# Kernel optimization log

Measured on AMD Instinct MI355X. Metric: run time of the kernel, lower is better.

Reference implementation:

```python
import jax, jax.numpy as jnp
import numpy as np

INPUT_SIZE = 2
HIDDEN = 64
NUM_CLASSES = 64
B = 4096
T = 512


def setup_inputs() -> dict:
    key = jax.random.key(0)
    ks = jax.random.split(key, 12)
    s_in = 1.0 / np.sqrt(HIDDEN)
    inp = {
        "x": jax.random.normal(ks[0], (B, INPUT_SIZE, T, 1), dtype=jnp.float32),
        # LSTMCell params (torch layout: [4H, in], gate order i,f,g,o)
        "W_ih": jax.random.uniform(ks[1], (4 * HIDDEN, INPUT_SIZE), minval=-s_in, maxval=s_in),
        "W_hh": jax.random.uniform(ks[2], (4 * HIDDEN, HIDDEN), minval=-s_in, maxval=s_in),
        "b_ih": jax.random.uniform(ks[3], (4 * HIDDEN,), minval=-s_in, maxval=s_in),
        "b_hh": jax.random.uniform(ks[4], (4 * HIDDEN,), minval=-s_in, maxval=s_in),
        # ODE cell f_node: Linear(H,H) -> Tanh -> Linear(H,H)
        "W1": jax.random.uniform(ks[5], (HIDDEN, HIDDEN), minval=-s_in, maxval=s_in),
        "b1": jax.random.uniform(ks[6], (HIDDEN,), minval=-s_in, maxval=s_in),
        "W2": jax.random.uniform(ks[7], (HIDDEN, HIDDEN), minval=-s_in, maxval=s_in),
        "b2": jax.random.uniform(ks[8], (HIDDEN,), minval=-s_in, maxval=s_in),
        # output projection fc
        "Wf": jax.random.uniform(ks[9], (NUM_CLASSES, HIDDEN), minval=-s_in, maxval=s_in),
        "bf": jax.random.uniform(ks[10], (NUM_CLASSES,), minval=-s_in, maxval=s_in),
    }
    return inp


def reference(x, W_ih, W_hh, b_ih, b_hh, W1, b1, W2, b2, Wf, bf):
    # x: [B, input_size, T, 1] -> [T, B, input_size] for scan over time
    xs = jnp.transpose(x[..., 0], (2, 0, 1))
    b = xs.shape[1]
    H = W_hh.shape[1]
    dt = jnp.float32(1.0 / 3.0)  # ts = ones(B), 3 fixed Euler steps of ts/3

    def f_node(h):
        return jnp.tanh(h @ W1.T + b1) @ W2.T + b2

    def step(carry, xt):
        h, c = carry
        gates = xt @ W_ih.T + h @ W_hh.T + (b_ih + b_hh)  # [B, 4H]
        i, f, g, o = jnp.split(gates, 4, axis=-1)
        c = jax.nn.sigmoid(f) * c + jax.nn.sigmoid(i) * jnp.tanh(g)
        h = jax.nn.sigmoid(o) * jnp.tanh(c)
        # fixed-Euler ODE solve: 3 steps
        for _ in range(3):
            h = h + dt * f_node(h)
        return (h, c), h @ Wf.T + bf

    h0 = jnp.zeros((b, H), dtype=x.dtype)
    c0 = jnp.zeros((b, H), dtype=x.dtype)
    _, outs = jax.lax.scan(step, (h0, c0), xs)  # outs: [T, B, num_classes]
    return jnp.transpose(outs, (1, 0, 2))  # [B, T, num_classes]
```

## Files before the change

kernel.cpp:

```cpp
#include <hip/hip_runtime.h>


#define TT 512
#define DT 0.33333334f

#define OFF_M  0
#define OFF_N  4096
#define OFF_P  20480
#define OFF_K1 24576
#define OFF_CG 24640
#define OFF_C2 24896

typedef _Float16 half8 __attribute__((ext_vector_type(8)));
typedef float f32x4 __attribute__((ext_vector_type(4)));

__device__ __forceinline__ float fsig(float x) {
  return __builtin_amdgcn_rcpf(1.0f + __expf(-x));
}
__device__ __forceinline__ float ftanh(float x) {
  return 2.0f * __builtin_amdgcn_rcpf(1.0f + __expf(-2.0f * x)) - 1.0f;
}

__global__ void prep(const float* __restrict__ Whh, const float* __restrict__ W1,
                     const float* __restrict__ W2, const float* __restrict__ b2,
                     const float* __restrict__ Wf, const float* __restrict__ bf,
                     float* __restrict__ ws) {
  int id = (int)blockIdx.x * 256 + (int)threadIdx.x;
  if (id < 4096) {
    int j = id >> 6, k = id & 63;
    float s = 0.f;
    for (int l = 0; l < 64; ++l) s += W1[j * 64 + l] * W2[l * 64 + k];
    ws[OFF_M + id] = DT * s;
  } else if (id < 20480) {
    int e = id - 4096; int gr = e >> 6, k = e & 63;
    float s = 0.f;
    for (int l = 0; l < 64; ++l) s += Whh[gr * 64 + l] * W2[l * 64 + k];
    ws[OFF_N + e] = DT * s;
  } else if (id < 24576) {
    int e = id - 20480; int j = e >> 6, k = e & 63;
    float s = 0.f;
    for (int l = 0; l < 64; ++l) s += Wf[j * 64 + l] * W2[l * 64 + k];
    ws[OFF_P + e] = DT * s;
  } else if (id < 24640) {
    int j = id - 24576;
    float s = 0.f;
    for (int l = 0; l < 64; ++l) s += W1[j * 64 + l] * b2[l];
    ws[OFF_K1 + j] = DT * s;
  } else if (id < 24896) {
    int gr = id - 24640;
    float s = 0.f;
    for (int l = 0; l < 64; ++l) s += Whh[gr * 64 + l] * b2[l];
    ws[OFF_CG + gr] = 3.0f * DT * s;
  } else if (id < 24960) {
    int j = id - 24896;
    float s = 0.f;
    for (int l = 0; l < 64; ++l) s += Wf[j * 64 + l] * b2[l];
    ws[OFF_C2 + j] = 3.0f * DT * s + bf[j];
  }
}

__device__ __forceinline__ half8 rdA(const _Float16* plane, int off) {
  return *(const half8*)(plane + off);
}

__global__ void __launch_bounds__(256, 2)
odelstm(const float* __restrict__ X, const float* __restrict__ Wih,
        const float* __restrict__ Whh, const float* __restrict__ bih,
        const float* __restrict__ bhh, const float* __restrict__ W1,
        const float* __restrict__ b1, const float* __restrict__ Wf,
        const float* __restrict__ ws, float* __restrict__ OUT)
{
  __shared__ __align__(16) _Float16 sh[5 * 1024];

  const int tid = (int)threadIdx.x;
  const int w = tid >> 6;
  const int l = tid & 63;
  const int q = l >> 4;
  const int p = l & 15;
  const int j = (w << 4) | p;
  const int row0 = (int)blockIdx.x << 3;

  half8 Bhh[4][2], Bw1[2], Bm[2], Bn[4][2], Bp[2], Bof[2];
  #pragma unroll
  for (int g = 0; g < 4; ++g) {
    #pragma unroll
    for (int kt = 0; kt < 2; ++kt) {
      const float* s  = Whh + ((g << 6) | j) * 64 + (kt << 5) + (q << 3);
      const float* sn = ws + OFF_N + (((g << 6) | j) << 6) + (kt << 5) + (q << 3);
      half8 v, vn;
      #pragma unroll
      for (int i = 0; i < 8; ++i) { v[i] = (_Float16)s[i]; vn[i] = (_Float16)sn[i]; }
      Bhh[g][kt] = v; Bn[g][kt] = vn;
    }
  }
  #pragma unroll
  for (int kt = 0; kt < 2; ++kt) {
    const float* s1 = W1 + j * 64 + (kt << 5) + (q << 3);
    const float* sm = ws + OFF_M + (j << 6) + (kt << 5) + (q << 3);
    const float* sp = ws + OFF_P + (j << 6) + (kt << 5) + (q << 3);
    const float* sf = Wf + j * 64 + (kt << 5) + (q << 3);
    half8 v1, vm, vp, vf;
    #pragma unroll
    for (int i = 0; i < 8; ++i) {
      v1[i] = (_Float16)s1[i]; vm[i] = (_Float16)sm[i];
      vp[i] = (_Float16)sp[i]; vf[i] = (_Float16)sf[i];
    }
    Bw1[kt] = v1; Bm[kt] = vm; Bp[kt] = vp; Bof[kt] = vf;
  }

  float bias0[4], biasL[4], wx0[4], wx1[4];
  #pragma unroll
  for (int g = 0; g < 4; ++g) {
    int gr = (g << 6) | j;
    bias0[g] = bih[gr] + bhh[gr];
    biasL[g] = bias0[g] + ws[OFF_CG + gr];
    wx0[g] = Wih[gr * 2];
    wx1[g] = Wih[gr * 2 + 1];
  }
  const float b1c = b1[j];
  const float k1c = ws[OFF_K1 + j];
  const float c2c = ws[OFF_C2 + j];

  int waddr[2];
  #pragma unroll
  for (int r = 0; r < 2; ++r) {
    int row = (q << 2) | r;
    waddr[r] = row * 64 + (((j >> 3) ^ (row & 7)) << 3) + (j & 7);
  }
  int roff0 = p * 64 + (((q) ^ (p & 7)) << 3);
  int roff1 = p * 64 + (((4 | q) ^ (p & 7)) << 3);

  const float* xp[2];
  float* outp[2];
  #pragma unroll
  for (int r = 0; r < 2; ++r) {
    int rb = row0 + ((q << 1) | r);
    xp[r]   = X + rb * 2 * TT;
    outp[r] = OUT + (rb * TT) * 64 + j;
  }

  for (int i = tid; i < 5 * 1024; i += 256) sh[i] = (_Float16)0.f;

  float x0[2], x1[2];
  #pragma unroll
  for (int r = 0; r < 2; ++r) { x0[r] = xp[r][0]; x1[r] = xp[r][TT]; }

  f32x4 acc[4];
  #pragma unroll
  for (int g = 0; g < 4; ++g) {
    acc[g][0] = bias0[g] + x0[0] * wx0[g] + x1[0] * wx1[g];
    acc[g][1] = bias0[g] + x0[1] * wx0[g] + x1[1] * wx1[g];
    acc[g][2] = 0.f; acc[g][3] = 0.f;
  }

  float c[2] = {0.f, 0.f};

  __syncthreads();

  for (int t = 0; t < TT; ++t) {
    _Float16* Hpl = sh + ((t & 1) << 10);
    _Float16* T0p = sh + 2048;
    _Float16* T1p = sh + 3072;
    _Float16* Spp = sh + 4096;

    #pragma unroll
    for (int r = 0; r < 2; ++r) {
      float ig = fsig(acc[0][r]);
      float fg = fsig(acc[1][r]);
      float gg = ftanh(acc[2][r]);
      float og = fsig(acc[3][r]);
      c[r] = fg * c[r] + ig * gg;
      float hv = og * ftanh(c[r]);
      Hpl[waddr[r]] = (_Float16)hv;
    }
    __syncthreads();

    half8 hf0 = rdA(Hpl, roff0);
    half8 hf1 = rdA(Hpl, roff1);
    f32x4 aa = {b1c, b1c, b1c, b1c};
    aa = __builtin_amdgcn_mfma_f32_16x16x32_f16(hf0, Bw1[0], aa, 0, 0, 0);
    aa = __builtin_amdgcn_mfma_f32_16x16x32_f16(hf1, Bw1[1], aa, 0, 0, 0);

    int tn = (t + 1 < TT) ? t + 1 : t;
    float nx0[2], nx1[2];
    #pragma unroll
    for (int r = 0; r < 2; ++r) { nx0[r] = xp[r][tn]; nx1[r] = xp[r][TT + tn]; }

    float t0s[2];
    #pragma unroll
    for (int r = 0; r < 2; ++r) {
      t0s[r] = ftanh(aa[r]);
      T0p[waddr[r]] = (_Float16)t0s[r];
    }
    __syncthreads();
    half8 t0f0 = rdA(T0p, roff0);
    half8 t0f1 = rdA(T0p, roff1);
    f32x4 a1 = {aa[0] + k1c, aa[1] + k1c, 0.f, 0.f};
    a1 = __builtin_amdgcn_mfma_f32_16x16x32_f16(t0f0, Bm[0], a1, 0, 0, 0);
    a1 = __builtin_amdgcn_mfma_f32_16x16x32_f16(t0f1, Bm[1], a1, 0, 0, 0);

    float t1s[2];
    #pragma unroll
    for (int r = 0; r < 2; ++r) {
      t1s[r] = ftanh(a1[r]);
      T1p[waddr[r]] = (_Float16)t1s[r];
    }
    __syncthreads();
    half8 t1f0 = rdA(T1p, roff0);
    half8 t1f1 = rdA(T1p, roff1);
    f32x4 a2 = {a1[0] + k1c, a1[1] + k1c, 0.f, 0.f};
    a2 = __builtin_amdgcn_mfma_f32_16x16x32_f16(t1f0, Bm[0], a2, 0, 0, 0);
    a2 = __builtin_amdgcn_mfma_f32_16x16x32_f16(t1f1, Bm[1], a2, 0, 0, 0);

    #pragma unroll
    for (int r = 0; r < 2; ++r) {
      float Sv = t0s[r] + t1s[r] + ftanh(a2[r]);
      Spp[waddr[r]] = (_Float16)Sv;
    }
    __syncthreads();

    half8 sf0 = rdA(Spp, roff0);
    half8 sf1 = rdA(Spp, roff1);

    #pragma unroll
    for (int g = 0; g < 4; ++g) {
      acc[g][0] = biasL[g] + nx0[0] * wx0[g] + nx1[0] * wx1[g];
      acc[g][1] = biasL[g] + nx0[1] * wx0[g] + nx1[1] * wx1[g];
      acc[g][2] = 0.f; acc[g][3] = 0.f;
      acc[g] = __builtin_amdgcn_mfma_f32_16x16x32_f16(hf0, Bhh[g][0], acc[g], 0, 0, 0);
      acc[g] = __builtin_amdgcn_mfma_f32_16x16x32_f16(hf1, Bhh[g][1], acc[g], 0, 0, 0);
      acc[g] = __builtin_amdgcn_mfma_f32_16x16x32_f16(sf0, Bn[g][0],  acc[g], 0, 0, 0);
      acc[g] = __builtin_amdgcn_mfma_f32_16x16x32_f16(sf1, Bn[g][1],  acc[g], 0, 0, 0);
    }

    f32x4 oa = {c2c, c2c, 0.f, 0.f};
    oa = __builtin_amdgcn_mfma_f32_16x16x32_f16(hf0, Bof[0], oa, 0, 0, 0);
    oa = __builtin_amdgcn_mfma_f32_16x16x32_f16(hf1, Bof[1], oa, 0, 0, 0);
    oa = __builtin_amdgcn_mfma_f32_16x16x32_f16(sf0, Bp[0],  oa, 0, 0, 0);
    oa = __builtin_amdgcn_mfma_f32_16x16x32_f16(sf1, Bp[1],  oa, 0, 0, 0);

    #pragma unroll
    for (int r = 0; r < 2; ++r) {
      outp[r][0] = oa[r];
      outp[r] += 64;
    }

    #pragma unroll
    for (int r = 0; r < 2; ++r) { x0[r] = nx0[r]; x1[r] = nx1[r]; }
  }
}

extern "C" void kernel_launch(void* const* d_in, const int* in_sizes, int n_in,
                              void* d_out, int out_size, void* d_ws, size_t ws_size,
                              hipStream_t stream) {
  const float* X   = (const float*)d_in[0];
  const float* Wih = (const float*)d_in[1];
  const float* Whh = (const float*)d_in[2];
  const float* bih = (const float*)d_in[3];
  const float* bhh = (const float*)d_in[4];
  const float* W1  = (const float*)d_in[5];
  const float* b1  = (const float*)d_in[6];
  const float* W2  = (const float*)d_in[7];
  const float* b2  = (const float*)d_in[8];
  const float* Wf  = (const float*)d_in[9];
  const float* bf  = (const float*)d_in[10];
  float* OUT = (float*)d_out;
  float* ws  = (float*)d_ws;

  hipLaunchKernelGGL(prep, dim3(98), dim3(256), 0, stream,
                     Whh, W1, W2, b2, Wf, bf, ws);

  int B = in_sizes[0] / (2 * TT);
  dim3 grid(B / 8), block(256);
  hipLaunchKernelGGL(odelstm, grid, block, 0, stream,
                     X, Wih, Whh, bih, bhh, W1, b1, Wf, ws, OUT);
}
```

Before: 1.076 ms.

## Halve batch rows per block to double grid size and occupancy

```diff
diff --git a/kernel.cpp b/kernel.cpp
--- a/kernel.cpp
+++ b/kernel.cpp
@@ -63,7 +63,7 @@
   return *(const half8*)(plane + off);
 }
 
-__global__ void __launch_bounds__(256, 2)
+__global__ void __launch_bounds__(256, 4)
 odelstm(const float* __restrict__ X, const float* __restrict__ Wih,
         const float* __restrict__ Whh, const float* __restrict__ bih,
         const float* __restrict__ bhh, const float* __restrict__ W1,
@@ -78,7 +78,7 @@
   const int q = l >> 4;
   const int p = l & 15;
   const int j = (w << 4) | p;
-  const int row0 = (int)blockIdx.x << 3;
+  const int row0 = (int)blockIdx.x << 2;
 
   half8 Bhh[4][2], Bw1[2], Bm[2], Bn[4][2], Bp[2], Bof[2];
   #pragma unroll
@@ -121,39 +121,27 @@
   const float k1c = ws[OFF_K1 + j];
   const float c2c = ws[OFF_C2 + j];
 
-  int waddr[2];
-  #pragma unroll
-  for (int r = 0; r < 2; ++r) {
-    int row = (q << 2) | r;
-    waddr[r] = row * 64 + (((j >> 3) ^ (row & 7)) << 3) + (j & 7);
-  }
-  int roff0 = p * 64 + (((q) ^ (p & 7)) << 3);
-  int roff1 = p * 64 + (((4 | q) ^ (p & 7)) << 3);
-
-  const float* xp[2];
-  float* outp[2];
-  #pragma unroll
-  for (int r = 0; r < 2; ++r) {
-    int rb = row0 + ((q << 1) | r);
-    xp[r]   = X + rb * 2 * TT;
-    outp[r] = OUT + (rb * TT) * 64 + j;
-  }
+  const int trow = q << 2;
+  const int waddr = trow * 64 + (((j >> 3) ^ (trow & 7)) << 3) + (j & 7);
+  const int roff0 = p * 64 + (((q) ^ (p & 7)) << 3);
+  const int roff1 = p * 64 + (((4 | q) ^ (p & 7)) << 3);
+
+  const int rb = row0 + q;
+  const float* xp = X + rb * 2 * TT;
+  float* outp = OUT + (rb * TT) * 64 + j;
 
   for (int i = tid; i < 5 * 1024; i += 256) sh[i] = (_Float16)0.f;
 
-  float x0[2], x1[2];
-  #pragma unroll
-  for (int r = 0; r < 2; ++r) { x0[r] = xp[r][0]; x1[r] = xp[r][TT]; }
+  float x0 = xp[0], x1 = xp[TT];
 
   f32x4 acc[4];
   #pragma unroll
   for (int g = 0; g < 4; ++g) {
-    acc[g][0] = bias0[g] + x0[0] * wx0[g] + x1[0] * wx1[g];
-    acc[g][1] = bias0[g] + x0[1] * wx0[g] + x1[1] * wx1[g];
-    acc[g][2] = 0.f; acc[g][3] = 0.f;
-  }
-
-  float c[2] = {0.f, 0.f};
+    acc[g][0] = bias0[g] + x0 * wx0[g] + x1 * wx1[g];
+    acc[g][1] = 0.f; acc[g][2] = 0.f; acc[g][3] = 0.f;
+  }
+
+  float c = 0.f;
 
   __syncthreads();
 
@@ -163,15 +151,14 @@
     _Float16* T1p = sh + 3072;
     _Float16* Spp = sh + 4096;
 
-    #pragma unroll
-    for (int r = 0; r < 2; ++r) {
-      float ig = fsig(acc[0][r]);
-      float fg = fsig(acc[1][r]);
-      float gg = ftanh(acc[2][r]);
-      float og = fsig(acc[3][r]);
-      c[r] = fg * c[r] + ig * gg;
-      float hv = og * ftanh(c[r]);
-      Hpl[waddr[r]] = (_Float16)hv;
+    {
+      float ig = fsig(acc[0][0]);
+      float fg = fsig(acc[1][0]);
+      float gg = ftanh(acc[2][0]);
+      float og = fsig(acc[3][0]);
+      c = fg * c + ig * gg;
+      float hv = og * ftanh(c);
+      Hpl[waddr] = (_Float16)hv;
     }
     __syncthreads();
 
@@ -182,40 +169,29 @@
     aa = __builtin_amdgcn_mfma_f32_16x16x32_f16(hf1, Bw1[1], aa, 0, 0, 0);
 
     int tn = (t + 1 < TT) ? t + 1 : t;
-    float nx0[2], nx1[2];
-    #pragma unroll
-    for (int r = 0; r < 2; ++r) { nx0[r] = xp[r][tn]; nx1[r] = xp[r][TT + tn]; }
-
-    float t0s[2];
-    #pragma unroll
-    for (int r = 0; r < 2; ++r) {
-      t0s[r] = ftanh(aa[r]);
-      T0p[waddr[r]] = (_Float16)t0s[r];
-    }
+    float nx0 = xp[tn], nx1 = xp[TT + tn];
+
+    float t0s = ftanh(aa[0]);
+    T0p[waddr] = (_Float16)t0s;
     __syncthreads();
     half8 t0f0 = rdA(T0p, roff0);
     half8 t0f1 = rdA(T0p, roff1);
-    f32x4 a1 = {aa[0] + k1c, aa[1] + k1c, 0.f, 0.f};
+    f32x4 a1 = {aa[0] + k1c, 0.f, 0.f, 0.f};
     a1 = __builtin_amdgcn_mfma_f32_16x16x32_f16(t0f0, Bm[0], a1, 0, 0, 0);
     a1 = __builtin_amdgcn_mfma_f32_16x16x32_f16(t0f1, Bm[1], a1, 0, 0, 0);
 
-    float t1s[2];
-    #pragma unroll
-    for (int r = 0; r < 2; ++r) {
-      t1s[r] = ftanh(a1[r]);
-      T1p[waddr[r]] = (_Float16)t1s[r];
-    }
+    float t1s = ftanh(a1[0]);
+    T1p[waddr] = (_Float16)t1s;
     __syncthreads();
     half8 t1f0 = rdA(T1p, roff0);
     half8 t1f1 = rdA(T1p, roff1);
-    f32x4 a2 = {a1[0] + k1c, a1[1] + k1c, 0.f, 0.f};
+    f32x4 a2 = {a1[0] + k1c, 0.f, 0.f, 0.f};
     a2 = __builtin_amdgcn_mfma_f32_16x16x32_f16(t1f0, Bm[0], a2, 0, 0, 0);
     a2 = __builtin_amdgcn_mfma_f32_16x16x32_f16(t1f1, Bm[1], a2, 0, 0, 0);
 
-    #pragma unroll
-    for (int r = 0; r < 2; ++r) {
-      float Sv = t0s[r] + t1s[r] + ftanh(a2[r]);
-      Spp[waddr[r]] = (_Float16)Sv;
+    {
+      float Sv = t0s + t1s + ftanh(a2[0]);
+      Spp[waddr] = (_Float16)Sv;
     }
     __syncthreads();
 
@@ -224,29 +200,24 @@
 
     #pragma unroll
     for (int g = 0; g < 4; ++g) {
-      acc[g][0] = biasL[g] + nx0[0] * wx0[g] + nx1[0] * wx1[g];
-      acc[g][1] = biasL[g] + nx0[1] * wx0[g] + nx1[1] * wx1[g];
-      acc[g][2] = 0.f; acc[g][3] = 0.f;
+      acc[g][0] = biasL[g] + nx0 * wx0[g] + nx1 * wx1[g];
+      acc[g][1] = 0.f; acc[g][2] = 0.f; acc[g][3] = 0.f;
       acc[g] = __builtin_amdgcn_mfma_f32_16x16x32_f16(hf0, Bhh[g][0], acc[g], 0, 0, 0);
       acc[g] = __builtin_amdgcn_mfma_f32_16x16x32_f16(hf1, Bhh[g][1], acc[g], 0, 0, 0);
       acc[g] = __builtin_amdgcn_mfma_f32_16x16x32_f16(sf0, Bn[g][0],  acc[g], 0, 0, 0);
       acc[g] = __builtin_amdgcn_mfma_f32_16x16x32_f16(sf1, Bn[g][1],  acc[g], 0, 0, 0);
     }
 
-    f32x4 oa = {c2c, c2c, 0.f, 0.f};
+    f32x4 oa = {c2c, 0.f, 0.f, 0.f};
     oa = __builtin_amdgcn_mfma_f32_16x16x32_f16(hf0, Bof[0], oa, 0, 0, 0);
     oa = __builtin_amdgcn_mfma_f32_16x16x32_f16(hf1, Bof[1], oa, 0, 0, 0);
     oa = __builtin_amdgcn_mfma_f32_16x16x32_f16(sf0, Bp[0],  oa, 0, 0, 0);
     oa = __builtin_amdgcn_mfma_f32_16x16x32_f16(sf1, Bp[1],  oa, 0, 0, 0);
 
-    #pragma unroll
-    for (int r = 0; r < 2; ++r) {
-      outp[r][0] = oa[r];
-      outp[r] += 64;
-    }
-
-    #pragma unroll
-    for (int r = 0; r < 2; ++r) { x0[r] = nx0[r]; x1[r] = nx1[r]; }
+    outp[0] = oa[0];
+    outp += 64;
+
+    x0 = nx0; x1 = nx1;
   }
 }
 
@@ -271,7 +242,7 @@
                      Whh, W1, W2, b2, Wf, bf, ws);
 
   int B = in_sizes[0] / (2 * TT);
-  dim3 grid(B / 8), block(256);
+  dim3 grid(B / 4), block(256);
   hipLaunchKernelGGL(odelstm, grid, block, 0, stream,
                      X, Wih, Whh, bih, bhh, W1, b1, Wf, ws, OUT);
 }
```

Result: slower. 2.988 ms (+177.8%).
